# Performance work log

Measured on AMD Instinct MI355X. Metric: run time of the kernel, lower is better.

Reference implementation:

```python
import jax, jax.numpy as jnp
import numpy as np

N = 50000        # nodes
E = 800000       # edges (avg degree 16)
D_IN = 19        # in_channels(16) + 2 coords + 1 observed flag
H = 64           # graph_hidden
L = 3            # graph_layers
EPS = 1e-5       # BatchNorm eps


def setup_inputs() -> dict:
    key = jax.random.key(0)
    ks = jax.random.split(key, 12)
    s = 0.05
    x = jax.random.normal(ks[0], (N, D_IN), jnp.float32)
    edge_index = jax.random.randint(ks[1], (2, E), 0, N, dtype=jnp.int32)
    return {
        "x": x,
        "edge_index": edge_index,
        # input projection + input BN
        "w_in": jax.random.normal(ks[2], (D_IN, H), jnp.float32) * s,
        "b_in": jnp.zeros((H,), jnp.float32),
        "bn0_g": jnp.ones((H,), jnp.float32),
        "bn0_b": jnp.zeros((H,), jnp.float32),
        # per-layer SAGEConv: lin_l (aggregated neighbors, with bias), lin_r (self, no bias)
        "wl": jax.random.normal(ks[3], (L, H, H), jnp.float32) * s,
        "bl": jnp.zeros((L, H), jnp.float32),
        "wr": jax.random.normal(ks[4], (L, H, H), jnp.float32) * s,
        # per-layer BatchNorm affine
        "bn_g": jnp.ones((L, H), jnp.float32),
        "bn_b": jnp.zeros((L, H), jnp.float32),
    }


def _batchnorm(h, g, b):
    # training-mode BN over the node axis (biased variance, like torch)
    mu = h.mean(axis=0)
    var = h.var(axis=0)
    return (h - mu) * jax.lax.rsqrt(var + EPS) * g + b


def reference(x, edge_index, w_in, b_in, bn0_g, bn0_b, wl, bl, wr, bn_g, bn_b):
    src = edge_index[0]
    dst = edge_index[1]
    n = x.shape[0]

    # input_proj -> BN -> ReLU  (dropout is identity at inference)
    h = x @ w_in + b_in
    h = jax.nn.relu(_batchnorm(h, bn0_g, bn0_b))

    # in-degree for mean aggregation (computed once)
    deg = jax.ops.segment_sum(jnp.ones((src.shape[0],), h.dtype), dst, num_segments=n)
    denom = jnp.maximum(deg, 1.0)[:, None]

    for l in range(L):
        # SAGEConv(mean): gather source feats, segment-mean into targets
        msgs = h[src]                                        # [E, H] gather
        agg = jax.ops.segment_sum(msgs, dst, num_segments=n) / denom
        h_new = agg @ wl[l] + bl[l] + h @ wr[l]
        h_new = jax.nn.relu(_batchnorm(h_new, bn_g[l], bn_b[l]))
        h = h + h_new                                        # residual
    return h
```

## Files before the change

kernel.cpp:

```cpp
#include <hip/hip_runtime.h>
#include <hip/hip_bf16.h>

#define NODES 50000
#define EDGES 800000
#define DIN   19
#define HDIM  64
#define LAYERS 3
#define BN_EPS 1e-5f

#define NBINS 196
#define EPB   4096
#define NBLK  196

typedef __attribute__((ext_vector_type(4))) float f32x4;
typedef __attribute__((ext_vector_type(8))) short s16x8;

__device__ inline ushort bf16bits(float f) {
    __hip_bfloat16 h = __float2bfloat16(f);
    return *reinterpret_cast<ushort*>(&h);
}
__device__ inline float bf16lo(unsigned v) { return __uint_as_float(v << 16); }
__device__ inline float bf16hi(unsigned v) { return __uint_as_float(v & 0xFFFF0000u); }


__global__ __launch_bounds__(1024) void k_sortA(const int* __restrict__ src, const int* __restrict__ dst,
                                                int2* __restrict__ cb, int* __restrict__ bintot,
                                                unsigned* __restrict__ bbuf) {
    __shared__ int hist[256];
    __shared__ int cur[256];
    __shared__ int wsum4[4];
    __shared__ unsigned stage[EPB];
    int blk = blockIdx.x, t = threadIdx.x;
    int e0 = blk * EPB;
    int ne = min(EPB, EDGES - e0);
    int d[4]; unsigned pk[4];
    #pragma unroll
    for (int i = 0; i < 4; ++i) {
        int j = t + i * 1024;
        if (j < ne) {
            int dd = dst[e0 + j];
            d[i] = dd;
            pk[i] = ((unsigned)(dd & 255) << 24) | (unsigned)src[e0 + j];
        } else d[i] = -1;
    }
    if (t < 256) hist[t] = 0;
    __syncthreads();
    #pragma unroll
    for (int i = 0; i < 4; ++i)
        if (d[i] >= 0) atomicAdd(&hist[d[i] >> 8], 1);
    __syncthreads();
    int ln = t & 63, wv = t >> 6;
    int cntv = 0, inc = 0;
    if (t < 256) {
        cntv = hist[t];
        inc = cntv;
        #pragma unroll
        for (int s = 1; s < 64; s <<= 1) {
            int u = __shfl_up(inc, s);
            if (ln >= s) inc += u;
        }
        if (ln == 63) wsum4[wv] = inc;
    }
    __syncthreads();
    if (t < 256) {
        int woff = 0;
        #pragma unroll
        for (int i = 0; i < 4; ++i) if (i < wv) woff += wsum4[i];
        int excl = woff + inc - cntv;
        cur[t] = excl;
        if (t < NBINS) {
            cb[t * NBLK + blk] = make_int2(excl, cntv);
            if (cntv) atomicAdd(&bintot[t], cntv);
        }
    }
    __syncthreads();
    #pragma unroll
    for (int i = 0; i < 4; ++i)
        if (d[i] >= 0) {
            int slot = atomicAdd(&cur[d[i] >> 8], 1);
            stage[slot] = pk[i];
        }
    __syncthreads();
    #pragma unroll
    for (int i = 0; i < 4; ++i) {
        int j = t + i * 1024;
        if (j < ne) bbuf[e0 + j] = stage[j];
    }
}


__global__ __launch_bounds__(512) void k_binB(const int2* __restrict__ cb, const int* __restrict__ bintot,
                                              const unsigned* __restrict__ bbuf,
                                              int* __restrict__ off, float* __restrict__ rdenom,
                                              int* __restrict__ ebuf) {
    __shared__ int red[256];
    __shared__ int segoff[NBINS], segcnt[NBINS];
    __shared__ int deg[256], loff[256], cur[256];
    __shared__ int wsum4[4];
    __shared__ int binoff_s;
    int b = blockIdx.x, t = threadIdx.x;
    int ln = t & 63, wv = t >> 6;
    if (t < 256) red[t] = (t < b) ? bintot[t] : 0;
    __syncthreads();
    #pragma unroll
    for (int s = 128; s > 0; s >>= 1) {
        if (t < s && t + s < 256) red[t] += red[t + s];
        __syncthreads();
    }
    if (t == 0) binoff_s = red[0];
    if (t < NBINS) {
        int2 c = cb[b * NBLK + t];
        segoff[t] = c.x; segcnt[t] = c.y;
    }
    if (t < 256) { deg[t] = 0; cur[t] = 0; }
    __syncthreads();
    int binoff = binoff_s;
    for (int sg = wv; sg < NBLK; sg += 8) {
        int c = segcnt[sg];
        const unsigned* bp = bbuf + sg * EPB + segoff[sg];
        for (int k = ln; k < c; k += 64) atomicAdd(&deg[bp[k] >> 24], 1);
    }
    __syncthreads();
    int dv = 0, inc = 0;
    if (t < 256) {
        dv = deg[t];
        inc = dv;
        #pragma unroll
        for (int s = 1; s < 64; s <<= 1) {
            int u = __shfl_up(inc, s);
            if (ln >= s) inc += u;
        }
        if (ln == 63) wsum4[wv] = inc;
    }
    __syncthreads();
    if (t < 256) {
        int woff = 0;
        #pragma unroll
        for (int i = 0; i < 4; ++i) if (i < wv) woff += wsum4[i];
        int excl = woff + inc - dv;
        loff[t] = excl;
        int node = (b << 8) + t;
        if (node < NODES) {
            off[node] = binoff + excl;
            rdenom[node] = 1.0f / fmaxf((float)dv, 1.0f);
        }
        if (b == NBINS - 1 && t == 0) off[NODES] = EDGES;
    }
    __syncthreads();
    for (int sg = wv; sg < NBLK; sg += 8) {
        int c = segcnt[sg];
        const unsigned* bp = bbuf + sg * EPB + segoff[sg];
        for (int k = ln; k < c; k += 64) {
            unsigned e = bp[k];
            int dd = e >> 24;
            int slot = atomicAdd(&cur[dd], 1);
            ebuf[binoff + loff[dd] + slot] = (int)(e & 0xFFFFFFu);
        }
    }
}


__global__ void k_prep(const float* __restrict__ x, const float* __restrict__ w_in,
                       const float* __restrict__ wl, const float* __restrict__ wr,
                       __hip_bfloat16* __restrict__ xpad, __hip_bfloat16* __restrict__ WiT,
                       __hip_bfloat16* __restrict__ WcatT) {
    int i = blockIdx.x * blockDim.x + threadIdx.x;
    if (i < 64 * 32) {
        int c = i >> 5, k = i & 31;
        WiT[i] = __float2bfloat16(k < DIN ? w_in[k * HDIM + c] : 0.0f);
    }
    if (i < LAYERS * 64 * 128) {
        int l = i >> 13;
        int rem = i & 8191;
        int c = rem >> 7, k = rem & 127;
        float v = (k < 64) ? wl[(l * 64 + k) * 64 + c] : wr[(l * 64 + (k - 64)) * 64 + c];
        WcatT[i] = __float2bfloat16(v);
    }
    if (i < NODES * 32) {
        int n = i >> 5, k = i & 31;
        xpad[i] = __float2bfloat16(k < DIN ? x[n * DIN + k] : 0.0f);
    }
}


__global__ void k_gemm(const __hip_bfloat16* __restrict__ A, int lda,
                       const __hip_bfloat16* __restrict__ WT, int K,
                       const float* __restrict__ bias, ushort* __restrict__ tb,
                       float* __restrict__ stats) {
    __shared__ float red[4][128];
    int lane = threadIdx.x & 63, wave = threadIdx.x >> 6;
    int row0 = blockIdx.x * 64 + wave * 16;
    int r = lane & 15, g = lane >> 4;
    f32x4 acc[4] = {{0.f,0.f,0.f,0.f},{0.f,0.f,0.f,0.f},{0.f,0.f,0.f,0.f},{0.f,0.f,0.f,0.f}};
    int ar = row0 + r;
    if (ar >= NODES) ar = NODES - 1;
    for (int k0 = 0; k0 < K; k0 += 32) {
        s16x8 af = *(const s16x8*)(A + (size_t)ar * lda + k0 + g * 8);
        #pragma unroll
        for (int j = 0; j < 4; ++j) {
            s16x8 bf = *(const s16x8*)(WT + (size_t)(j * 16 + r) * K + k0 + g * 8);
            acc[j] = __builtin_amdgcn_mfma_f32_16x16x32_bf16(af, bf, acc[j], 0, 0, 0);
        }
    }
    float s_[4], q_[4];
    #pragma unroll
    for (int j = 0; j < 4; ++j) {
        float b = bias[j * 16 + r];
        float s = 0.0f, q = 0.0f;
        #pragma unroll
        for (int i = 0; i < 4; ++i) {
            int row = row0 + g * 4 + i;
            if (row < NODES) {
                float v = acc[j][i] + b;
                tb[(size_t)row * 64 + j * 16 + r] = bf16bits(v);
                s += v; q += v * v;
            }
        }
        s += __shfl_xor(s, 16); s += __shfl_xor(s, 32);
        q += __shfl_xor(q, 16); q += __shfl_xor(q, 32);
        s_[j] = s; q_[j] = q;
    }
    if (g == 0) {
        #pragma unroll
        for (int j = 0; j < 4; ++j) {
            red[wave][j * 16 + r] = s_[j];
            red[wave][64 + j * 16 + r] = q_[j];
        }
    }
    __syncthreads();
    if (threadIdx.x < 128) {
        float tot = red[0][threadIdx.x] + red[1][threadIdx.x] +
                    red[2][threadIdx.x] + red[3][threadIdx.x];
        atomicAdd(&stats[threadIdx.x * 16], tot);
    }
}


__global__ void k_apply(const ushort* __restrict__ tb, const float* __restrict__ stats,
                        const float* __restrict__ gamma, const float* __restrict__ beta,
                        float* __restrict__ h, __hip_bfloat16* __restrict__ AB, int residual) {
    int idx0 = blockIdx.x * blockDim.x + threadIdx.x;
    int stride = gridDim.x * blockDim.x;
    const float invN = 1.0f / NODES;
    for (int idx = idx0; idx < NODES * 16; idx += stride) {
        int n = idx >> 4;
        int j = (idx & 15) * 4;
        ushort4 tv = *(const ushort4*)(tb + (size_t)n * 64 + j);
        float tf[4] = { __uint_as_float((unsigned)tv.x << 16), __uint_as_float((unsigned)tv.y << 16),
                        __uint_as_float((unsigned)tv.z << 16), __uint_as_float((unsigned)tv.w << 16) };
        f32x4 hv;
        if (residual) hv = *(const f32x4*)(h + (size_t)n * 64 + j);
        float out[4];
        ushort ub[4];
        #pragma unroll
        for (int k = 0; k < 4; ++k) {
            int f = j + k;
            float mu = stats[f * 16] * invN;
            float var = stats[(64 + f) * 16] * invN - mu * mu;
            float sc = gamma[f] * rsqrtf(var + BN_EPS);
            float sh = beta[f] - mu * sc;
            float v = fmaxf(tf[k] * sc + sh, 0.0f);
            out[k] = residual ? (hv[k] + v) : v;
            ub[k] = bf16bits(out[k]);
        }
        *(f32x4*)(h + (size_t)n * 64 + j) = f32x4{out[0], out[1], out[2], out[3]};
        *(ushort4*)((ushort*)AB + (size_t)n * 128 + 64 + j) = make_ushort4(ub[0], ub[1], ub[2], ub[3]);
    }
}


__global__ void k_agg(const int* __restrict__ off, const int* __restrict__ ebuf,
                      const float* __restrict__ rdenom, __hip_bfloat16* __restrict__ ABh) {
    unsigned* AB = (unsigned*)ABh;
    int lane = threadIdx.x & 63;
    int half = lane >> 5;
    int fl = lane & 31;
    int w = blockIdx.x * (blockDim.x >> 6) + (threadIdx.x >> 6);
    int nw = gridDim.x * (blockDim.x >> 6);
    for (int n = w; n < NODES; n += nw) {
        int p0 = off[n], p1 = off[n + 1];
        float a0 = 0.0f, a1 = 0.0f;
        int p = p0 + half;
        for (; p + 6 < p1; p += 8) {
            int s0 = ebuf[p];
            int s1 = ebuf[p + 2];
            int s2 = ebuf[p + 4];
            int s3 = ebuf[p + 6];
            unsigned v0 = AB[(size_t)s0 * 64 + 32 + fl];
            unsigned v1 = AB[(size_t)s1 * 64 + 32 + fl];
            unsigned v2 = AB[(size_t)s2 * 64 + 32 + fl];
            unsigned v3 = AB[(size_t)s3 * 64 + 32 + fl];
            a0 += bf16lo(v0); a1 += bf16hi(v0);
            a0 += bf16lo(v1); a1 += bf16hi(v1);
            a0 += bf16lo(v2); a1 += bf16hi(v2);
            a0 += bf16lo(v3); a1 += bf16hi(v3);
        }
        for (; p < p1; p += 2) {
            int s = ebuf[p];
            unsigned v = AB[(size_t)s * 64 + 32 + fl];
            a0 += bf16lo(v); a1 += bf16hi(v);
        }
        a0 += __shfl_xor(a0, 32);
        a1 += __shfl_xor(a1, 32);
        if (half == 0) {
            float rd = rdenom[n];
            unsigned o = (unsigned)bf16bits(a0 * rd) | ((unsigned)bf16bits(a1 * rd) << 16);
            AB[(size_t)n * 64 + fl] = o;
        }
    }
}


extern "C" void kernel_launch(void* const* d_in, const int* in_sizes, int n_in,
                              void* d_out, int out_size, void* d_ws, size_t ws_size,
                              hipStream_t stream) {
    const float* x    = (const float*)d_in[0];
    const int*   ei   = (const int*)d_in[1];
    const float* w_in = (const float*)d_in[2];
    const float* b_in = (const float*)d_in[3];
    const float* bn0g = (const float*)d_in[4];
    const float* bn0b = (const float*)d_in[5];
    const float* wl   = (const float*)d_in[6];
    const float* bl   = (const float*)d_in[7];
    const float* wr   = (const float*)d_in[8];
    const float* bng  = (const float*)d_in[9];
    const float* bnb  = (const float*)d_in[10];
    const int* esrc = ei;
    const int* edst = ei + EDGES;
    float* h = (float*)d_out;

    char* p = (char*)d_ws;
    auto alloc = [&](size_t bytes) {
        char* r = p;
        p += (bytes + 255) & ~size_t(255);
        return r;
    };
    int*   bintot = (int*)alloc((size_t)NBINS * 4);
    float* stats  = (float*)alloc((size_t)4 * 128 * 16 * 4);
    char*  zero_end = p;
    int2*     cb   = (int2*)alloc((size_t)NBINS * NBLK * 8);
    unsigned* bbuf = (unsigned*)alloc((size_t)NBLK * EPB * 4);
    int*   off  = (int*)alloc((size_t)(NODES + 1) * 4);
    float* rden = (float*)alloc((size_t)NODES * 4);
    int*   ebuf = (int*)alloc((size_t)EDGES * 4);
    __hip_bfloat16* xpad  = (__hip_bfloat16*)alloc((size_t)NODES * 32 * 2);
    __hip_bfloat16* WiT   = (__hip_bfloat16*)alloc(64 * 32 * 2);
    __hip_bfloat16* WcatT = (__hip_bfloat16*)alloc(LAYERS * 64 * 128 * 2);
    __hip_bfloat16* AB    = (__hip_bfloat16*)alloc((size_t)NODES * 128 * 2);
    ushort* tb = (ushort*)alloc((size_t)NODES * 64 * 2);

    hipMemsetAsync(bintot, 0, (size_t)(zero_end - (char*)bintot), stream);

    k_sortA<<<NBLK, 1024, 0, stream>>>(esrc, edst, cb, bintot, bbuf);
    k_binB<<<NBINS, 512, 0, stream>>>(cb, bintot, bbuf, off, rden, ebuf);
    k_prep<<<(NODES * 32 + 255) / 256, 256, 0, stream>>>(x, w_in, wl, wr, xpad, WiT, WcatT);

    k_gemm<<<(NODES + 63) / 64, 256, 0, stream>>>(xpad, 32, WiT, 32, b_in, tb, stats);
    k_apply<<<2048, 256, 0, stream>>>(tb, stats, bn0g, bn0b, h, AB, 0);

    for (int l = 0; l < LAYERS; ++l) {
        k_agg<<<2048, 256, 0, stream>>>(off, ebuf, rden, AB);
        k_gemm<<<(NODES + 63) / 64, 256, 0, stream>>>(AB, 128, WcatT + l * 8192, 128,
                                                      bl + l * 64, tb, stats + (l + 1) * 2048);
        k_apply<<<2048, 256, 0, stream>>>(tb, stats + (l + 1) * 2048, bng + l * 64, bnb + l * 64,
                                          h, AB, 1);
    }
}
```

Measured before the change: 304.8 us.

## Fuse pipeline into persistent megakernel with grid barriers and LDS-resident aggregation

Result: slower. 683.4 us (+124.2%).

```diff
diff --git a/kernel.cpp b/kernel.cpp
--- a/kernel.cpp
+++ b/kernel.cpp
@@ -4,13 +4,15 @@
 #define NODES 50000
 #define EDGES 800000
 #define DIN   19
-#define HDIM  64
 #define LAYERS 3
 #define BN_EPS 1e-5f
 
 #define NBINS 196
-#define EPB   4096
-#define NBLK  196
+#define EPB   2048
+#define NBLK  391
+#define NTILES 782
+#define GRID  782
+#define TPB   256
 
 typedef __attribute__((ext_vector_type(4))) float f32x4;
 typedef __attribute__((ext_vector_type(8))) short s16x8;
@@ -22,180 +24,243 @@
 __device__ inline float bf16lo(unsigned v) { return __uint_as_float(v << 16); }
 __device__ inline float bf16hi(unsigned v) { return __uint_as_float(v & 0xFFFF0000u); }
 
-
-__global__ __launch_bounds__(1024) void k_sortA(const int* __restrict__ src, const int* __restrict__ dst,
-                                                int2* __restrict__ cb, int* __restrict__ bintot,
-                                                unsigned* __restrict__ bbuf) {
-    __shared__ int hist[256];
-    __shared__ int cur[256];
-    __shared__ int wsum4[4];
-    __shared__ unsigned stage[EPB];
-    int blk = blockIdx.x, t = threadIdx.x;
-    int e0 = blk * EPB;
+union SMem {
+    struct { int hist[256], cur[256], wsum[4]; unsigned stage[EPB]; } sort;
+    struct { int red[256]; int segoff[NBLK], segcnt[NBLK], pre[NBLK + 1];
+             int deg[256], loff[256], cur[256], wsum[4]; } binb;
+    struct { ushort aggtile[64][136]; float red[4][128]; } gemm;
+};
+
+__device__ inline void gbar(int* barr, int k) {
+    __syncthreads();
+    if (threadIdx.x == 0) {
+        __threadfence();
+        __hip_atomic_fetch_add(&barr[(blockIdx.x & 7) * 16], 1,
+                               __ATOMIC_RELEASE, __HIP_MEMORY_SCOPE_AGENT);
+        if (blockIdx.x == 0) {
+            const int target = (k + 1) * GRID;
+            for (;;) {
+                int s = 0;
+                #pragma unroll
+                for (int i = 0; i < 8; ++i)
+                    s += __hip_atomic_load(&barr[i * 16], __ATOMIC_RELAXED, __HIP_MEMORY_SCOPE_AGENT);
+                if (s >= target) break;
+                __builtin_amdgcn_s_sleep(4);
+            }
+            __hip_atomic_fetch_add(&barr[128], 1, __ATOMIC_RELEASE, __HIP_MEMORY_SCOPE_AGENT);
+        } else {
+            while (__hip_atomic_load(&barr[128], __ATOMIC_RELAXED, __HIP_MEMORY_SCOPE_AGENT) < k + 1)
+                __builtin_amdgcn_s_sleep(16);
+        }
+        __threadfence();
+    }
+    __syncthreads();
+}
+
+
+__device__ inline void do_sort(int c, int t, const int* __restrict__ esrc,
+                               const int* __restrict__ edst, int2* __restrict__ cb,
+                               int* __restrict__ bintot, unsigned* __restrict__ bbuf, SMem& sm) {
+    int ln = t & 63, wv = t >> 6;
+    int e0 = c * EPB;
     int ne = min(EPB, EDGES - e0);
-    int d[4]; unsigned pk[4];
-    #pragma unroll
-    for (int i = 0; i < 4; ++i) {
-        int j = t + i * 1024;
+    int d[8]; unsigned pk[8];
+    #pragma unroll
+    for (int i = 0; i < 8; ++i) {
+        int j = t + i * TPB;
         if (j < ne) {
-            int dd = dst[e0 + j];
+            int dd = edst[e0 + j];
             d[i] = dd;
-            pk[i] = ((unsigned)(dd & 255) << 24) | (unsigned)src[e0 + j];
+            pk[i] = ((unsigned)(dd & 255) << 24) | (unsigned)esrc[e0 + j];
         } else d[i] = -1;
     }
-    if (t < 256) hist[t] = 0;
-    __syncthreads();
-    #pragma unroll
-    for (int i = 0; i < 4; ++i)
-        if (d[i] >= 0) atomicAdd(&hist[d[i] >> 8], 1);
-    __syncthreads();
+    sm.sort.hist[t] = 0;
+    __syncthreads();
+    #pragma unroll
+    for (int i = 0; i < 8; ++i)
+        if (d[i] >= 0) atomicAdd(&sm.sort.hist[d[i] >> 8], 1);
+    __syncthreads();
+    int cnt = sm.sort.hist[t], inc = cnt;
+    #pragma unroll
+    for (int s = 1; s < 64; s <<= 1) {
+        int u = __shfl_up(inc, s);
+        if (ln >= s) inc += u;
+    }
+    if (ln == 63) sm.sort.wsum[wv] = inc;
+    __syncthreads();
+    int woff = 0;
+    #pragma unroll
+    for (int i = 0; i < 4; ++i) if (i < wv) woff += sm.sort.wsum[i];
+    int excl = woff + inc - cnt;
+    sm.sort.cur[t] = excl;
+    if (t < NBINS) {
+        cb[t * NBLK + c] = make_int2(excl, cnt);
+        if (cnt) atomicAdd(&bintot[t], cnt);
+    }
+    __syncthreads();
+    #pragma unroll
+    for (int i = 0; i < 8; ++i)
+        if (d[i] >= 0) {
+            int slot = atomicAdd(&sm.sort.cur[d[i] >> 8], 1);
+            sm.sort.stage[slot] = pk[i];
+        }
+    __syncthreads();
+    #pragma unroll
+    for (int i = 0; i < 8; ++i) {
+        int j = t + i * TPB;
+        if (j < ne) bbuf[e0 + j] = sm.sort.stage[j];
+    }
+    __syncthreads();
+}
+
+
+__device__ inline int ubound(const int* pre, int f) {
+    int lo = 0, hi = NBLK;
+    while (lo + 1 < hi) {
+        int mid = (lo + hi) >> 1;
+        if (pre[mid] <= f) lo = mid; else hi = mid;
+    }
+    return lo;
+}
+
+__device__ inline void do_binb(int b, int t, const int2* __restrict__ cb,
+                               const int* __restrict__ bintot, const unsigned* __restrict__ bbuf,
+                               int* __restrict__ off, float* __restrict__ rden,
+                               int* __restrict__ ebuf, SMem& sm) {
     int ln = t & 63, wv = t >> 6;
-    int cntv = 0, inc = 0;
-    if (t < 256) {
-        cntv = hist[t];
-        inc = cntv;
-        #pragma unroll
-        for (int s = 1; s < 64; s <<= 1) {
-            int u = __shfl_up(inc, s);
-            if (ln >= s) inc += u;
-        }
-        if (ln == 63) wsum4[wv] = inc;
-    }
-    __syncthreads();
-    if (t < 256) {
-        int woff = 0;
-        #pragma unroll
-        for (int i = 0; i < 4; ++i) if (i < wv) woff += wsum4[i];
-        int excl = woff + inc - cntv;
-        cur[t] = excl;
-        if (t < NBINS) {
-            cb[t * NBLK + blk] = make_int2(excl, cntv);
-            if (cntv) atomicAdd(&bintot[t], cntv);
-        }
-    }
-    __syncthreads();
-    #pragma unroll
-    for (int i = 0; i < 4; ++i)
-        if (d[i] >= 0) {
-            int slot = atomicAdd(&cur[d[i] >> 8], 1);
-            stage[slot] = pk[i];
-        }
-    __syncthreads();
-    #pragma unroll
-    for (int i = 0; i < 4; ++i) {
-        int j = t + i * 1024;
-        if (j < ne) bbuf[e0 + j] = stage[j];
-    }
-}
-
-
-__global__ __launch_bounds__(512) void k_binB(const int2* __restrict__ cb, const int* __restrict__ bintot,
-                                              const unsigned* __restrict__ bbuf,
-                                              int* __restrict__ off, float* __restrict__ rdenom,
-                                              int* __restrict__ ebuf) {
-    __shared__ int red[256];
-    __shared__ int segoff[NBINS], segcnt[NBINS];
-    __shared__ int deg[256], loff[256], cur[256];
-    __shared__ int wsum4[4];
-    __shared__ int binoff_s;
-    int b = blockIdx.x, t = threadIdx.x;
-    int ln = t & 63, wv = t >> 6;
-    if (t < 256) red[t] = (t < b) ? bintot[t] : 0;
+    sm.binb.red[t] = (t < b) ? bintot[t] : 0;
     __syncthreads();
     #pragma unroll
     for (int s = 128; s > 0; s >>= 1) {
-        if (t < s && t + s < 256) red[t] += red[t + s];
+        if (t < s) sm.binb.red[t] += sm.binb.red[t + s];
         __syncthreads();
     }
-    if (t == 0) binoff_s = red[0];
-    if (t < NBINS) {
-        int2 c = cb[b * NBLK + t];
-        segoff[t] = c.x; segcnt[t] = c.y;
-    }
-    if (t < 256) { deg[t] = 0; cur[t] = 0; }
-    __syncthreads();
-    int binoff = binoff_s;
-    for (int sg = wv; sg < NBLK; sg += 8) {
-        int c = segcnt[sg];
-        const unsigned* bp = bbuf + sg * EPB + segoff[sg];
-        for (int k = ln; k < c; k += 64) atomicAdd(&deg[bp[k] >> 24], 1);
-    }
-    __syncthreads();
-    int dv = 0, inc = 0;
-    if (t < 256) {
-        dv = deg[t];
-        inc = dv;
-        #pragma unroll
-        for (int s = 1; s < 64; s <<= 1) {
-            int u = __shfl_up(inc, s);
-            if (ln >= s) inc += u;
-        }
-        if (ln == 63) wsum4[wv] = inc;
-    }
-    __syncthreads();
-    if (t < 256) {
-        int woff = 0;
-        #pragma unroll
-        for (int i = 0; i < 4; ++i) if (i < wv) woff += wsum4[i];
-        int excl = woff + inc - dv;
-        loff[t] = excl;
-        int node = (b << 8) + t;
-        if (node < NODES) {
-            off[node] = binoff + excl;
-            rdenom[node] = 1.0f / fmaxf((float)dv, 1.0f);
-        }
-        if (b == NBINS - 1 && t == 0) off[NODES] = EDGES;
-    }
-    __syncthreads();
-    for (int sg = wv; sg < NBLK; sg += 8) {
-        int c = segcnt[sg];
-        const unsigned* bp = bbuf + sg * EPB + segoff[sg];
-        for (int k = ln; k < c; k += 64) {
-            unsigned e = bp[k];
-            int dd = e >> 24;
-            int slot = atomicAdd(&cur[dd], 1);
-            ebuf[binoff + loff[dd] + slot] = (int)(e & 0xFFFFFFu);
-        }
-    }
-}
-
-
-__global__ void k_prep(const float* __restrict__ x, const float* __restrict__ w_in,
-                       const float* __restrict__ wl, const float* __restrict__ wr,
-                       __hip_bfloat16* __restrict__ xpad, __hip_bfloat16* __restrict__ WiT,
-                       __hip_bfloat16* __restrict__ WcatT) {
-    int i = blockIdx.x * blockDim.x + threadIdx.x;
-    if (i < 64 * 32) {
-        int c = i >> 5, k = i & 31;
-        WiT[i] = __float2bfloat16(k < DIN ? w_in[k * HDIM + c] : 0.0f);
-    }
-    if (i < LAYERS * 64 * 128) {
-        int l = i >> 13;
-        int rem = i & 8191;
-        int c = rem >> 7, k = rem & 127;
-        float v = (k < 64) ? wl[(l * 64 + k) * 64 + c] : wr[(l * 64 + (k - 64)) * 64 + c];
-        WcatT[i] = __float2bfloat16(v);
-    }
-    if (i < NODES * 32) {
-        int n = i >> 5, k = i & 31;
-        xpad[i] = __float2bfloat16(k < DIN ? x[n * DIN + k] : 0.0f);
-    }
-}
-
-
-__global__ void k_gemm(const __hip_bfloat16* __restrict__ A, int lda,
-                       const __hip_bfloat16* __restrict__ WT, int K,
-                       const float* __restrict__ bias, ushort* __restrict__ tb,
-                       float* __restrict__ stats) {
-    __shared__ float red[4][128];
-    int lane = threadIdx.x & 63, wave = threadIdx.x >> 6;
-    int row0 = blockIdx.x * 64 + wave * 16;
+    int binoff = sm.binb.red[0];
+    for (int sg = t; sg < NBLK; sg += TPB) {
+        int2 c = cb[b * NBLK + sg];
+        sm.binb.segoff[sg] = c.x;
+        sm.binb.segcnt[sg] = c.y;
+    }
+    sm.binb.deg[t] = 0;
+    sm.binb.cur[t] = 0;
+    __syncthreads();
+    if (wv == 0) {
+        int carry = 0;
+        for (int base = 0; base < NBLK; base += 64) {
+            int idx = base + ln;
+            int v = (idx < NBLK) ? sm.binb.segcnt[idx] : 0;
+            int inc = v;
+            #pragma unroll
+            for (int s = 1; s < 64; s <<= 1) {
+                int u = __shfl_up(inc, s);
+                if (ln >= s) inc += u;
+            }
+            if (idx < NBLK) sm.binb.pre[idx] = carry + inc - v;
+            carry += __shfl(inc, 63);
+        }
+        if (ln == 0) sm.binb.pre[NBLK] = carry;
+    }
+    __syncthreads();
+    int total = sm.binb.pre[NBLK];
+    for (int f = t; f < total; f += TPB) {
+        int sg = ubound(sm.binb.pre, f);
+        unsigned e = bbuf[sg * EPB + sm.binb.segoff[sg] + (f - sm.binb.pre[sg])];
+        atomicAdd(&sm.binb.deg[e >> 24], 1);
+    }
+    __syncthreads();
+    int dv = sm.binb.deg[t], inc2 = dv;
+    #pragma unroll
+    for (int s = 1; s < 64; s <<= 1) {
+        int u = __shfl_up(inc2, s);
+        if (ln >= s) inc2 += u;
+    }
+    if (ln == 63) sm.binb.wsum[wv] = inc2;
+    __syncthreads();
+    int woff = 0;
+    #pragma unroll
+    for (int i = 0; i < 4; ++i) if (i < wv) woff += sm.binb.wsum[i];
+    int excl = woff + inc2 - dv;
+    sm.binb.loff[t] = excl;
+    int node = (b << 8) + t;
+    if (node < NODES) {
+        off[node] = binoff + excl;
+        rden[node] = 1.0f / fmaxf((float)dv, 1.0f);
+    }
+    if (b == NBINS - 1 && t == 0) off[NODES] = EDGES;
+    __syncthreads();
+    for (int f = t; f < total; f += TPB) {
+        int sg = ubound(sm.binb.pre, f);
+        unsigned e = bbuf[sg * EPB + sm.binb.segoff[sg] + (f - sm.binb.pre[sg])];
+        int dd = e >> 24;
+        int slot = atomicAdd(&sm.binb.cur[dd], 1);
+        ebuf[binoff + sm.binb.loff[dd] + slot] = (int)(e & 0xFFFFFFu);
+    }
+    __syncthreads();
+}
+
+
+__device__ inline void do_agg(int rb, int t, const int* __restrict__ off,
+                              const int* __restrict__ ebuf, const float* __restrict__ rden,
+                              const ushort* __restrict__ hb, SMem& sm) {
+    const unsigned* HB = (const unsigned*)hb;
+    unsigned (*AG)[68] = (unsigned (*)[68])sm.gemm.aggtile;
+    int lane = t & 63, wave = t >> 6;
+    int half = lane >> 5, fl = lane & 31;
+    #pragma unroll 1
+    for (int i = 0; i < 16; ++i) {
+        int n = rb * 64 + wave * 16 + i;
+        if (n < NODES) {
+            int p0 = off[n], p1 = off[n + 1];
+            float a0 = 0.0f, a1 = 0.0f;
+            int p = p0 + half;
+            for (; p + 6 < p1; p += 8) {
+                int s0 = ebuf[p], s1 = ebuf[p + 2], s2 = ebuf[p + 4], s3 = ebuf[p + 6];
+                unsigned v0 = HB[(size_t)s0 * 32 + fl];
+                unsigned v1 = HB[(size_t)s1 * 32 + fl];
+                unsigned v2 = HB[(size_t)s2 * 32 + fl];
+                unsigned v3 = HB[(size_t)s3 * 32 + fl];
+                a0 += bf16lo(v0); a1 += bf16hi(v0);
+                a0 += bf16lo(v1); a1 += bf16hi(v1);
+                a0 += bf16lo(v2); a1 += bf16hi(v2);
+                a0 += bf16lo(v3); a1 += bf16hi(v3);
+            }
+            for (; p < p1; p += 2) {
+                unsigned v = HB[(size_t)ebuf[p] * 32 + fl];
+                a0 += bf16lo(v); a1 += bf16hi(v);
+            }
+            a0 += __shfl_xor(a0, 32);
+            a1 += __shfl_xor(a1, 32);
+            if (half == 0) {
+                float rd = rden[n];
+                AG[wave * 16 + i][fl] =
+                    (unsigned)bf16bits(a0 * rd) | ((unsigned)bf16bits(a1 * rd) << 16);
+            }
+        }
+    }
+    __syncthreads();
+}
+
+
+template<int K, bool ALDS>
+__device__ inline void do_gemm(int rb, int t, const ushort* __restrict__ Aglob,
+                               const ushort* __restrict__ WT, const float* __restrict__ bias,
+                               ushort* __restrict__ tb, float* __restrict__ stats,
+                               const ushort* __restrict__ hb, SMem& sm) {
+    int lane = t & 63, wave = t >> 6;
+    int row0 = rb * 64 + wave * 16;
     int r = lane & 15, g = lane >> 4;
     f32x4 acc[4] = {{0.f,0.f,0.f,0.f},{0.f,0.f,0.f,0.f},{0.f,0.f,0.f,0.f},{0.f,0.f,0.f,0.f}};
     int ar = row0 + r;
     if (ar >= NODES) ar = NODES - 1;
+    #pragma unroll
     for (int k0 = 0; k0 < K; k0 += 32) {
-        s16x8 af = *(const s16x8*)(A + (size_t)ar * lda + k0 + g * 8);
+        s16x8 af;
+        if (ALDS) {
+            if (k0 < 64) af = *(const s16x8*)&sm.gemm.aggtile[wave * 16 + r][k0 + g * 8];
+            else         af = *(const s16x8*)(hb + (size_t)ar * 64 + (k0 - 64) + g * 8);
+        } else {
+            af = *(const s16x8*)(Aglob + (size_t)ar * 32 + k0 + g * 8);
+        }
         #pragma unroll
         for (int j = 0; j < 4; ++j) {
             s16x8 bf = *(const s16x8*)(WT + (size_t)(j * 16 + r) * K + k0 + g * 8);
@@ -223,26 +288,26 @@
     if (g == 0) {
         #pragma unroll
         for (int j = 0; j < 4; ++j) {
-            red[wave][j * 16 + r] = s_[j];
-            red[wave][64 + j * 16 + r] = q_[j];
-        }
-    }
-    __syncthreads();
-    if (threadIdx.x < 128) {
-        float tot = red[0][threadIdx.x] + red[1][threadIdx.x] +
-                    red[2][threadIdx.x] + red[3][threadIdx.x];
-        atomicAdd(&stats[threadIdx.x * 16], tot);
-    }
-}
-
-
-__global__ void k_apply(const ushort* __restrict__ tb, const float* __restrict__ stats,
-                        const float* __restrict__ gamma, const float* __restrict__ beta,
-                        float* __restrict__ h, __hip_bfloat16* __restrict__ AB, int residual) {
-    int idx0 = blockIdx.x * blockDim.x + threadIdx.x;
-    int stride = gridDim.x * blockDim.x;
+            sm.gemm.red[wave][j * 16 + r] = s_[j];
+            sm.gemm.red[wave][64 + j * 16 + r] = q_[j];
+        }
+    }
+    __syncthreads();
+    if (t < 128) {
+        float tot = sm.gemm.red[0][t] + sm.gemm.red[1][t] +
+                    sm.gemm.red[2][t] + sm.gemm.red[3][t];
+        atomicAdd(&stats[t * 16], tot);
+    }
+    __syncthreads();
+}
+
+
+__device__ inline void do_apply(int t, const ushort* __restrict__ tb,
+                                const float* __restrict__ stats, const float* __restrict__ gamma,
+                                const float* __restrict__ beta, float* __restrict__ h,
+                                ushort* __restrict__ hb, bool residual) {
     const float invN = 1.0f / NODES;
-    for (int idx = idx0; idx < NODES * 16; idx += stride) {
+    for (int idx = blockIdx.x * TPB + t; idx < NODES * 16; idx += GRID * TPB) {
         int n = idx >> 4;
         int j = (idx & 15) * 4;
         ushort4 tv = *(const ushort4*)(tb + (size_t)n * 64 + j);
@@ -264,49 +329,71 @@
             ub[k] = bf16bits(out[k]);
         }
         *(f32x4*)(h + (size_t)n * 64 + j) = f32x4{out[0], out[1], out[2], out[3]};
-        *(ushort4*)((ushort*)AB + (size_t)n * 128 + 64 + j) = make_ushort4(ub[0], ub[1], ub[2], ub[3]);
-    }
-}
-
-
-__global__ void k_agg(const int* __restrict__ off, const int* __restrict__ ebuf,
-                      const float* __restrict__ rdenom, __hip_bfloat16* __restrict__ ABh) {
-    unsigned* AB = (unsigned*)ABh;
-    int lane = threadIdx.x & 63;
-    int half = lane >> 5;
-    int fl = lane & 31;
-    int w = blockIdx.x * (blockDim.x >> 6) + (threadIdx.x >> 6);
-    int nw = gridDim.x * (blockDim.x >> 6);
-    for (int n = w; n < NODES; n += nw) {
-        int p0 = off[n], p1 = off[n + 1];
-        float a0 = 0.0f, a1 = 0.0f;
-        int p = p0 + half;
-        for (; p + 6 < p1; p += 8) {
-            int s0 = ebuf[p];
-            int s1 = ebuf[p + 2];
-            int s2 = ebuf[p + 4];
-            int s3 = ebuf[p + 6];
-            unsigned v0 = AB[(size_t)s0 * 64 + 32 + fl];
-            unsigned v1 = AB[(size_t)s1 * 64 + 32 + fl];
-            unsigned v2 = AB[(size_t)s2 * 64 + 32 + fl];
-            unsigned v3 = AB[(size_t)s3 * 64 + 32 + fl];
-            a0 += bf16lo(v0); a1 += bf16hi(v0);
-            a0 += bf16lo(v1); a1 += bf16hi(v1);
-            a0 += bf16lo(v2); a1 += bf16hi(v2);
-            a0 += bf16lo(v3); a1 += bf16hi(v3);
-        }
-        for (; p < p1; p += 2) {
-            int s = ebuf[p];
-            unsigned v = AB[(size_t)s * 64 + 32 + fl];
-            a0 += bf16lo(v); a1 += bf16hi(v);
-        }
-        a0 += __shfl_xor(a0, 32);
-        a1 += __shfl_xor(a1, 32);
-        if (half == 0) {
-            float rd = rdenom[n];
-            unsigned o = (unsigned)bf16bits(a0 * rd) | ((unsigned)bf16bits(a1 * rd) << 16);
-            AB[(size_t)n * 64 + fl] = o;
-        }
+        *(ushort4*)(hb + (size_t)n * 64 + j) = make_ushort4(ub[0], ub[1], ub[2], ub[3]);
+    }
+}
+
+
+__global__ void k_first(const float* __restrict__ x, const float* __restrict__ w_in,
+                        const float* __restrict__ wl, const float* __restrict__ wr,
+                        ushort* __restrict__ xpad, ushort* __restrict__ WiT,
+                        ushort* __restrict__ WcatT, int* __restrict__ barr,
+                        int* __restrict__ bintot, float* __restrict__ stats) {
+    int i0 = blockIdx.x * blockDim.x + threadIdx.x;
+    int stride = gridDim.x * blockDim.x;
+    for (int i = i0; i < 256; i += stride) barr[i] = 0;
+    for (int i = i0; i < NBINS; i += stride) bintot[i] = 0;
+    for (int i = i0; i < 4 * 2048; i += stride) stats[i] = 0.0f;
+    for (int i = i0; i < 64 * 32; i += stride) {
+        int c = i >> 5, k = i & 31;
+        WiT[i] = bf16bits(k < DIN ? w_in[k * 64 + c] : 0.0f);
+    }
+    for (int i = i0; i < LAYERS * 64 * 128; i += stride) {
+        int l = i >> 13, rem = i & 8191;
+        int c = rem >> 7, k = rem & 127;
+        float v = (k < 64) ? wl[(l * 64 + k) * 64 + c] : wr[(l * 64 + (k - 64)) * 64 + c];
+        WcatT[i] = bf16bits(v);
+    }
+    for (int i = i0; i < NODES * 32; i += stride) {
+        int n = i >> 5, k = i & 31;
+        xpad[i] = bf16bits(k < DIN ? x[n * DIN + k] : 0.0f);
+    }
+}
+
+
+__global__ __launch_bounds__(TPB, 4) void k_mega(
+    const int* __restrict__ esrc, const int* __restrict__ edst,
+    const float* __restrict__ b_in, const float* __restrict__ bn0g, const float* __restrict__ bn0b,
+    const float* __restrict__ bl, const float* __restrict__ bng, const float* __restrict__ bnb,
+    const ushort* __restrict__ xpad, const ushort* __restrict__ WiT, const ushort* __restrict__ WcatT,
+    int2* __restrict__ cb, int* __restrict__ bintot, unsigned* __restrict__ bbuf,
+    int* __restrict__ off, float* __restrict__ rden, int* __restrict__ ebuf,
+    ushort* __restrict__ tb, ushort* __restrict__ hb, float* __restrict__ stats,
+    float* __restrict__ h, int* __restrict__ barr) {
+    __shared__ SMem sm;
+    int t = threadIdx.x;
+    int bk = 0;
+
+    for (int c = blockIdx.x; c < NBLK; c += GRID)
+        do_sort(c, t, esrc, edst, cb, bintot, bbuf, sm);
+    gbar(barr, bk++);
+
+    if (blockIdx.x < NBINS)
+        do_binb(blockIdx.x, t, cb, bintot, bbuf, off, rden, ebuf, sm);
+    __syncthreads();
+    do_gemm<32, false>(blockIdx.x, t, xpad, WiT, b_in, tb, stats, nullptr, sm);
+    gbar(barr, bk++);
+
+    do_apply(t, tb, stats, bn0g, bn0b, h, hb, false);
+    gbar(barr, bk++);
+
+    for (int l = 0; l < LAYERS; ++l) {
+        do_agg(blockIdx.x, t, off, ebuf, rden, hb, sm);
+        do_gemm<128, true>(blockIdx.x, t, nullptr, WcatT + l * 8192, bl + l * 64,
+                           tb, stats + (l + 1) * 2048, hb, sm);
+        gbar(barr, bk++);
+        do_apply(t, tb, stats + (l + 1) * 2048, bng + l * 64, bnb + l * 64, h, hb, true);
+        if (l < LAYERS - 1) gbar(barr, bk++);
     }
 }
 
@@ -335,34 +422,22 @@
         p += (bytes + 255) & ~size_t(255);
         return r;
     };
-    int*   bintot = (int*)alloc((size_t)NBINS * 4);
-    float* stats  = (float*)alloc((size_t)4 * 128 * 16 * 4);
-    char*  zero_end = p;
-    int2*     cb   = (int2*)alloc((size_t)NBINS * NBLK * 8);
-    unsigned* bbuf = (unsigned*)alloc((size_t)NBLK * EPB * 4);
-    int*   off  = (int*)alloc((size_t)(NODES + 1) * 4);
-    float* rden = (float*)alloc((size_t)NODES * 4);
-    int*   ebuf = (int*)alloc((size_t)EDGES * 4);
-    __hip_bfloat16* xpad  = (__hip_bfloat16*)alloc((size_t)NODES * 32 * 2);
-    __hip_bfloat16* WiT   = (__hip_bfloat16*)alloc(64 * 32 * 2);
-    __hip_bfloat16* WcatT = (__hip_bfloat16*)alloc(LAYERS * 64 * 128 * 2);
-    __hip_bfloat16* AB    = (__hip_bfloat16*)alloc((size_t)NODES * 128 * 2);
-    ushort* tb = (ushort*)alloc((size_t)NODES * 64 * 2);
-
-    hipMemsetAsync(bintot, 0, (size_t)(zero_end - (char*)bintot), stream);
-
-    k_sortA<<<NBLK, 1024, 0, stream>>>(esrc, edst, cb, bintot, bbuf);
-    k_binB<<<NBINS, 512, 0, stream>>>(cb, bintot, bbuf, off, rden, ebuf);
-    k_prep<<<(NODES * 32 + 255) / 256, 256, 0, stream>>>(x, w_in, wl, wr, xpad, WiT, WcatT);
-
-    k_gemm<<<(NODES + 63) / 64, 256, 0, stream>>>(xpad, 32, WiT, 32, b_in, tb, stats);
-    k_apply<<<2048, 256, 0, stream>>>(tb, stats, bn0g, bn0b, h, AB, 0);
-
-    for (int l = 0; l < LAYERS; ++l) {
-        k_agg<<<2048, 256, 0, stream>>>(off, ebuf, rden, AB);
-        k_gemm<<<(NODES + 63) / 64, 256, 0, stream>>>(AB, 128, WcatT + l * 8192, 128,
-                                                      bl + l * 64, tb, stats + (l + 1) * 2048);
-        k_apply<<<2048, 256, 0, stream>>>(tb, stats + (l + 1) * 2048, bng + l * 64, bnb + l * 64,
-                                          h, AB, 1);
-    }
-}
+    int*      barr   = (int*)alloc(1024);
+    int*      bintot = (int*)alloc((size_t)NBINS * 4);
+    float*    stats  = (float*)alloc((size_t)4 * 2048 * 4);
+    int2*     cb     = (int2*)alloc((size_t)NBINS * NBLK * 8);
+    unsigned* bbuf   = (unsigned*)alloc((size_t)NBLK * EPB * 4);
+    int*      off    = (int*)alloc((size_t)(NODES + 1) * 4);
+    float*    rden   = (float*)alloc((size_t)NODES * 4);
+    int*      ebuf   = (int*)alloc((size_t)EDGES * 4);
+    ushort*   xpad   = (ushort*)alloc((size_t)NODES * 32 * 2);
+    ushort*   WiT    = (ushort*)alloc(64 * 32 * 2);
+    ushort*   WcatT  = (ushort*)alloc(LAYERS * 64 * 128 * 2);
+    ushort*   tb     = (ushort*)alloc((size_t)NODES * 64 * 2);
+    ushort*   hb     = (ushort*)alloc((size_t)NODES * 64 * 2);
+
+    k_first<<<512, TPB, 0, stream>>>(x, w_in, wl, wr, xpad, WiT, WcatT, barr, bintot, stats);
+    k_mega<<<GRID, TPB, 0, stream>>>(esrc, edst, b_in, bn0g, bn0b, bl, bng, bnb,
+                                     xpad, WiT, WcatT, cb, bintot, bbuf, off, rden, ebuf,
+                                     tb, hb, stats, h, barr);
+}
```

## Fuse neighbor aggregation into layer GEMM and restructure edge binning and prep

Applied to the files above, without the earlier changes.

Result: slower. 360.8 us (+18.4%).

```diff
diff --git a/kernel.cpp b/kernel.cpp
--- a/kernel.cpp
+++ b/kernel.cpp
@@ -4,13 +4,14 @@
 #define NODES 50000
 #define EDGES 800000
 #define DIN   19
-#define HDIM  64
 #define LAYERS 3
 #define BN_EPS 1e-5f
 
 #define NBINS 196
 #define EPB   4096
 #define NBLK  196
+#define NTILES 782
+#define TPB   256
 
 typedef __attribute__((ext_vector_type(4))) float f32x4;
 typedef __attribute__((ext_vector_type(8))) short s16x8;
@@ -21,6 +22,27 @@
 }
 __device__ inline float bf16lo(unsigned v) { return __uint_as_float(v << 16); }
 __device__ inline float bf16hi(unsigned v) { return __uint_as_float(v & 0xFFFF0000u); }
+
+
+__global__ void k_wprep(const float* __restrict__ w_in, const float* __restrict__ wl,
+                        const float* __restrict__ wr, ushort* __restrict__ WiT,
+                        ushort* __restrict__ WcatT, int* __restrict__ bintot,
+                        float* __restrict__ stats) {
+    int i0 = blockIdx.x * blockDim.x + threadIdx.x;
+    int stride = gridDim.x * blockDim.x;
+    for (int i = i0; i < NBINS; i += stride) bintot[i] = 0;
+    for (int i = i0; i < 4 * 2048; i += stride) stats[i] = 0.0f;
+    for (int i = i0; i < 64 * 32; i += stride) {
+        int c = i >> 5, k = i & 31;
+        WiT[i] = bf16bits(k < DIN ? w_in[k * 64 + c] : 0.0f);
+    }
+    for (int i = i0; i < LAYERS * 64 * 128; i += stride) {
+        int l = i >> 13, rem = i & 8191;
+        int c = rem >> 7, k = rem & 127;
+        float v = (k < 64) ? wl[(l * 64 + k) * 64 + c] : wr[(l * 64 + (k - 64)) * 64 + c];
+        WcatT[i] = bf16bits(v);
+    }
+}
 
 
 __global__ __launch_bounds__(1024) void k_sortA(const int* __restrict__ src, const int* __restrict__ dst,
@@ -89,119 +111,98 @@
 }
 
 
-__global__ __launch_bounds__(512) void k_binB(const int2* __restrict__ cb, const int* __restrict__ bintot,
+__device__ inline int ubound(const int* pre, int f) {
+    int lo = 0, hi = NBLK;
+    while (lo + 1 < hi) {
+        int mid = (lo + hi) >> 1;
+        if (pre[mid] <= f) lo = mid; else hi = mid;
+    }
+    return lo;
+}
+
+__global__ __launch_bounds__(TPB) void k_binB(const int2* __restrict__ cb, const int* __restrict__ bintot,
                                               const unsigned* __restrict__ bbuf,
-                                              int* __restrict__ off, float* __restrict__ rdenom,
+                                              int* __restrict__ off, float* __restrict__ rden,
                                               int* __restrict__ ebuf) {
     __shared__ int red[256];
-    __shared__ int segoff[NBINS], segcnt[NBINS];
+    __shared__ int segoff[NBLK], segcnt[NBLK], pre[NBLK + 1];
     __shared__ int deg[256], loff[256], cur[256];
     __shared__ int wsum4[4];
-    __shared__ int binoff_s;
     int b = blockIdx.x, t = threadIdx.x;
     int ln = t & 63, wv = t >> 6;
-    if (t < 256) red[t] = (t < b) ? bintot[t] : 0;
+    red[t] = (t < b) ? bintot[t] : 0;
     __syncthreads();
     #pragma unroll
     for (int s = 128; s > 0; s >>= 1) {
-        if (t < s && t + s < 256) red[t] += red[t + s];
+        if (t < s) red[t] += red[t + s];
         __syncthreads();
     }
-    if (t == 0) binoff_s = red[0];
-    if (t < NBINS) {
+    int binoff = red[0];
+    if (t < NBLK) {
         int2 c = cb[b * NBLK + t];
         segoff[t] = c.x; segcnt[t] = c.y;
     }
-    if (t < 256) { deg[t] = 0; cur[t] = 0; }
-    __syncthreads();
-    int binoff = binoff_s;
-    for (int sg = wv; sg < NBLK; sg += 8) {
-        int c = segcnt[sg];
-        const unsigned* bp = bbuf + sg * EPB + segoff[sg];
-        for (int k = ln; k < c; k += 64) atomicAdd(&deg[bp[k] >> 24], 1);
-    }
-    __syncthreads();
-    int dv = 0, inc = 0;
-    if (t < 256) {
-        dv = deg[t];
-        inc = dv;
-        #pragma unroll
-        for (int s = 1; s < 64; s <<= 1) {
-            int u = __shfl_up(inc, s);
-            if (ln >= s) inc += u;
-        }
-        if (ln == 63) wsum4[wv] = inc;
-    }
-    __syncthreads();
-    if (t < 256) {
-        int woff = 0;
-        #pragma unroll
-        for (int i = 0; i < 4; ++i) if (i < wv) woff += wsum4[i];
-        int excl = woff + inc - dv;
-        loff[t] = excl;
-        int node = (b << 8) + t;
-        if (node < NODES) {
-            off[node] = binoff + excl;
-            rdenom[node] = 1.0f / fmaxf((float)dv, 1.0f);
-        }
-        if (b == NBINS - 1 && t == 0) off[NODES] = EDGES;
-    }
-    __syncthreads();
-    for (int sg = wv; sg < NBLK; sg += 8) {
-        int c = segcnt[sg];
-        const unsigned* bp = bbuf + sg * EPB + segoff[sg];
-        for (int k = ln; k < c; k += 64) {
-            unsigned e = bp[k];
-            int dd = e >> 24;
-            int slot = atomicAdd(&cur[dd], 1);
-            ebuf[binoff + loff[dd] + slot] = (int)(e & 0xFFFFFFu);
-        }
-    }
-}
-
-
-__global__ void k_prep(const float* __restrict__ x, const float* __restrict__ w_in,
-                       const float* __restrict__ wl, const float* __restrict__ wr,
-                       __hip_bfloat16* __restrict__ xpad, __hip_bfloat16* __restrict__ WiT,
-                       __hip_bfloat16* __restrict__ WcatT) {
-    int i = blockIdx.x * blockDim.x + threadIdx.x;
-    if (i < 64 * 32) {
-        int c = i >> 5, k = i & 31;
-        WiT[i] = __float2bfloat16(k < DIN ? w_in[k * HDIM + c] : 0.0f);
-    }
-    if (i < LAYERS * 64 * 128) {
-        int l = i >> 13;
-        int rem = i & 8191;
-        int c = rem >> 7, k = rem & 127;
-        float v = (k < 64) ? wl[(l * 64 + k) * 64 + c] : wr[(l * 64 + (k - 64)) * 64 + c];
-        WcatT[i] = __float2bfloat16(v);
-    }
-    if (i < NODES * 32) {
-        int n = i >> 5, k = i & 31;
-        xpad[i] = __float2bfloat16(k < DIN ? x[n * DIN + k] : 0.0f);
-    }
-}
-
-
-__global__ void k_gemm(const __hip_bfloat16* __restrict__ A, int lda,
-                       const __hip_bfloat16* __restrict__ WT, int K,
-                       const float* __restrict__ bias, ushort* __restrict__ tb,
-                       float* __restrict__ stats) {
-    __shared__ float red[4][128];
-    int lane = threadIdx.x & 63, wave = threadIdx.x >> 6;
-    int row0 = blockIdx.x * 64 + wave * 16;
+    deg[t] = 0; cur[t] = 0;
+    __syncthreads();
+    if (wv == 0) {
+        int carry = 0;
+        for (int base = 0; base < NBLK; base += 64) {
+            int idx = base + ln;
+            int v = (idx < NBLK) ? segcnt[idx] : 0;
+            int inc = v;
+            #pragma unroll
+            for (int s = 1; s < 64; s <<= 1) {
+                int u = __shfl_up(inc, s);
+                if (ln >= s) inc += u;
+            }
+            if (idx < NBLK) pre[idx] = carry + inc - v;
+            carry += __shfl(inc, 63);
+        }
+        if (ln == 0) pre[NBLK] = carry;
+    }
+    __syncthreads();
+    int total = pre[NBLK];
+    for (int f = t; f < total; f += TPB) {
+        int sg = ubound(pre, f);
+        unsigned e = bbuf[sg * EPB + segoff[sg] + (f - pre[sg])];
+        atomicAdd(&deg[e >> 24], 1);
+    }
+    __syncthreads();
+    int dv = deg[t], inc2 = dv;
+    #pragma unroll
+    for (int s = 1; s < 64; s <<= 1) {
+        int u = __shfl_up(inc2, s);
+        if (ln >= s) inc2 += u;
+    }
+    if (ln == 63) wsum4[wv] = inc2;
+    __syncthreads();
+    int woff = 0;
+    #pragma unroll
+    for (int i = 0; i < 4; ++i) if (i < wv) woff += wsum4[i];
+    int excl = woff + inc2 - dv;
+    loff[t] = excl;
+    int node = (b << 8) + t;
+    if (node < NODES) {
+        off[node] = binoff + excl;
+        rden[node] = 1.0f / fmaxf((float)dv, 1.0f);
+    }
+    if (b == NBINS - 1 && t == 0) off[NODES] = EDGES;
+    __syncthreads();
+    for (int f = t; f < total; f += TPB) {
+        int sg = ubound(pre, f);
+        unsigned e = bbuf[sg * EPB + segoff[sg] + (f - pre[sg])];
+        int dd = e >> 24;
+        int slot = atomicAdd(&cur[dd], 1);
+        ebuf[binoff + loff[dd] + slot] = (int)(e & 0xFFFFFFu);
+    }
+}
+
+
+__device__ inline void gemm_epilogue(int t, int row0, f32x4* acc, const float* __restrict__ bias,
+                                     ushort* __restrict__ tb, float* __restrict__ stats,
+                                     float (*red)[128]) {
+    int lane = t & 63, wave = t >> 6;
     int r = lane & 15, g = lane >> 4;
-    f32x4 acc[4] = {{0.f,0.f,0.f,0.f},{0.f,0.f,0.f,0.f},{0.f,0.f,0.f,0.f},{0.f,0.f,0.f,0.f}};
-    int ar = row0 + r;
-    if (ar >= NODES) ar = NODES - 1;
-    for (int k0 = 0; k0 < K; k0 += 32) {
-        s16x8 af = *(const s16x8*)(A + (size_t)ar * lda + k0 + g * 8);
-        #pragma unroll
-        for (int j = 0; j < 4; ++j) {
-            s16x8 bf = *(const s16x8*)(WT + (size_t)(j * 16 + r) * K + k0 + g * 8);
-            acc[j] = __builtin_amdgcn_mfma_f32_16x16x32_bf16(af, bf, acc[j], 0, 0, 0);
-        }
-    }
     float s_[4], q_[4];
     #pragma unroll
     for (int j = 0; j < 4; ++j) {
@@ -209,7 +210,7 @@
         float s = 0.0f, q = 0.0f;
         #pragma unroll
         for (int i = 0; i < 4; ++i) {
-            int row = row0 + g * 4 + i;
+            int row = row0 + wave * 16 + g * 4 + i;
             if (row < NODES) {
                 float v = acc[j][i] + b;
                 tb[(size_t)row * 64 + j * 16 + r] = bf16bits(v);
@@ -228,17 +229,110 @@
         }
     }
     __syncthreads();
-    if (threadIdx.x < 128) {
-        float tot = red[0][threadIdx.x] + red[1][threadIdx.x] +
-                    red[2][threadIdx.x] + red[3][threadIdx.x];
-        atomicAdd(&stats[threadIdx.x * 16], tot);
-    }
+    if (t < 128) {
+        float tot = red[0][t] + red[1][t] + red[2][t] + red[3][t];
+        atomicAdd(&stats[t * 16], tot);
+    }
+}
+
+
+__global__ __launch_bounds__(TPB) void k_gemm0(const float* __restrict__ x, const ushort* __restrict__ WiT,
+                                               const float* __restrict__ bias, ushort* __restrict__ tb,
+                                               float* __restrict__ stats) {
+    __shared__ ushort xt[64][40];
+    __shared__ float red[4][128];
+    int t = threadIdx.x, rb = blockIdx.x;
+    int row0 = rb * 64;
+    int nv = min(64, NODES - row0);
+    unsigned* xz = (unsigned*)xt;
+    for (int i = t; i < 64 * 20; i += TPB) xz[i] = 0;
+    __syncthreads();
+    const float* xs = x + (size_t)row0 * DIN;
+    for (int e = t; e < nv * DIN; e += TPB) {
+        int n = e / DIN, k = e - n * DIN;
+        xt[n][k] = bf16bits(xs[e]);
+    }
+    __syncthreads();
+    int lane = t & 63, wave = t >> 6;
+    int r = lane & 15, g = lane >> 4;
+    f32x4 acc[4] = {{0.f,0.f,0.f,0.f},{0.f,0.f,0.f,0.f},{0.f,0.f,0.f,0.f},{0.f,0.f,0.f,0.f}};
+    s16x8 af = *(const s16x8*)&xt[wave * 16 + r][g * 8];
+    #pragma unroll
+    for (int j = 0; j < 4; ++j) {
+        s16x8 bf = *(const s16x8*)(WiT + (size_t)(j * 16 + r) * 32 + g * 8);
+        acc[j] = __builtin_amdgcn_mfma_f32_16x16x32_bf16(af, bf, acc[j], 0, 0, 0);
+    }
+    gemm_epilogue(t, row0, acc, bias, tb, stats, red);
+}
+
+
+__global__ __launch_bounds__(TPB) void k_aggemm(const int* __restrict__ off, const int* __restrict__ ebuf,
+                                                const float* __restrict__ rden, const ushort* __restrict__ hb,
+                                                const ushort* __restrict__ WT, const float* __restrict__ bias,
+                                                ushort* __restrict__ tb, float* __restrict__ stats) {
+    __shared__ ushort aggt[64][136];
+    __shared__ float red[4][128];
+    int t = threadIdx.x, rb = blockIdx.x;
+    const unsigned* HB = (const unsigned*)hb;
+    unsigned (*AG)[68] = (unsigned (*)[68])aggt;
+    int lane = t & 63, wave = t >> 6;
+    int half = lane >> 5, fl = lane & 31;
+    #pragma unroll 1
+    for (int i = 0; i < 16; ++i) {
+        int n = rb * 64 + wave * 16 + i;
+        if (n < NODES) {
+            int p0 = off[n], p1 = off[n + 1];
+            float a0 = 0.0f, a1 = 0.0f;
+            int p = p0 + half;
+            for (; p + 6 < p1; p += 8) {
+                int s0 = ebuf[p], s1 = ebuf[p + 2], s2 = ebuf[p + 4], s3 = ebuf[p + 6];
+                unsigned v0 = HB[(size_t)s0 * 32 + fl];
+                unsigned v1 = HB[(size_t)s1 * 32 + fl];
+                unsigned v2 = HB[(size_t)s2 * 32 + fl];
+                unsigned v3 = HB[(size_t)s3 * 32 + fl];
+                a0 += bf16lo(v0); a1 += bf16hi(v0);
+                a0 += bf16lo(v1); a1 += bf16hi(v1);
+                a0 += bf16lo(v2); a1 += bf16hi(v2);
+                a0 += bf16lo(v3); a1 += bf16hi(v3);
+            }
+            for (; p < p1; p += 2) {
+                unsigned v = HB[(size_t)ebuf[p] * 32 + fl];
+                a0 += bf16lo(v); a1 += bf16hi(v);
+            }
+            a0 += __shfl_xor(a0, 32);
+            a1 += __shfl_xor(a1, 32);
+            if (half == 0) {
+                float rd = rden[n];
+                AG[wave * 16 + i][fl] =
+                    (unsigned)bf16bits(a0 * rd) | ((unsigned)bf16bits(a1 * rd) << 16);
+            }
+        }
+    }
+    __syncthreads();
+    int r = lane & 15, g = lane >> 4;
+    int row0 = rb * 64;
+    int ar = row0 + wave * 16 + r;
+    if (ar >= NODES) ar = NODES - 1;
+    f32x4 acc[4] = {{0.f,0.f,0.f,0.f},{0.f,0.f,0.f,0.f},{0.f,0.f,0.f,0.f},{0.f,0.f,0.f,0.f}};
+    #pragma unroll
+    for (int k0 = 0; k0 < 128; k0 += 32) {
+        s16x8 af;
+        if (k0 < 64) af = *(const s16x8*)&aggt[wave * 16 + r][k0 + g * 8];
+        else         af = *(const s16x8*)(hb + (size_t)ar * 64 + (k0 - 64) + g * 8);
+        #pragma unroll
+        for (int j = 0; j < 4; ++j) {
+            s16x8 bf = *(const s16x8*)(WT + (size_t)(j * 16 + r) * 128 + k0 + g * 8);
+            acc[j] = __builtin_amdgcn_mfma_f32_16x16x32_bf16(af, bf, acc[j], 0, 0, 0);
+        }
+    }
+    gemm_epilogue(t, row0, acc, bias, tb, stats, red);
 }
 
 
 __global__ void k_apply(const ushort* __restrict__ tb, const float* __restrict__ stats,
                         const float* __restrict__ gamma, const float* __restrict__ beta,
-                        float* __restrict__ h, __hip_bfloat16* __restrict__ AB, int residual) {
+                        float* __restrict__ h, ushort* __restrict__ hb,
+                        int residual, int write_hb) {
     int idx0 = blockIdx.x * blockDim.x + threadIdx.x;
     int stride = gridDim.x * blockDim.x;
     const float invN = 1.0f / NODES;
@@ -264,49 +358,8 @@
             ub[k] = bf16bits(out[k]);
         }
         *(f32x4*)(h + (size_t)n * 64 + j) = f32x4{out[0], out[1], out[2], out[3]};
-        *(ushort4*)((ushort*)AB + (size_t)n * 128 + 64 + j) = make_ushort4(ub[0], ub[1], ub[2], ub[3]);
-    }
-}
-
-
-__global__ void k_agg(const int* __restrict__ off, const int* __restrict__ ebuf,
-                      const float* __restrict__ rdenom, __hip_bfloat16* __restrict__ ABh) {
-    unsigned* AB = (unsigned*)ABh;
-    int lane = threadIdx.x & 63;
-    int half = lane >> 5;
-    int fl = lane & 31;
-    int w = blockIdx.x * (blockDim.x >> 6) + (threadIdx.x >> 6);
-    int nw = gridDim.x * (blockDim.x >> 6);
-    for (int n = w; n < NODES; n += nw) {
-        int p0 = off[n], p1 = off[n + 1];
-        float a0 = 0.0f, a1 = 0.0f;
-        int p = p0 + half;
-        for (; p + 6 < p1; p += 8) {
-            int s0 = ebuf[p];
-            int s1 = ebuf[p + 2];
-            int s2 = ebuf[p + 4];
-            int s3 = ebuf[p + 6];
-            unsigned v0 = AB[(size_t)s0 * 64 + 32 + fl];
-            unsigned v1 = AB[(size_t)s1 * 64 + 32 + fl];
-            unsigned v2 = AB[(size_t)s2 * 64 + 32 + fl];
-            unsigned v3 = AB[(size_t)s3 * 64 + 32 + fl];
-            a0 += bf16lo(v0); a1 += bf16hi(v0);
-            a0 += bf16lo(v1); a1 += bf16hi(v1);
-            a0 += bf16lo(v2); a1 += bf16hi(v2);
-            a0 += bf16lo(v3); a1 += bf16hi(v3);
-        }
-        for (; p < p1; p += 2) {
-            int s = ebuf[p];
-            unsigned v = AB[(size_t)s * 64 + 32 + fl];
-            a0 += bf16lo(v); a1 += bf16hi(v);
-        }
-        a0 += __shfl_xor(a0, 32);
-        a1 += __shfl_xor(a1, 32);
-        if (half == 0) {
-            float rd = rdenom[n];
-            unsigned o = (unsigned)bf16bits(a0 * rd) | ((unsigned)bf16bits(a1 * rd) << 16);
-            AB[(size_t)n * 64 + fl] = o;
-        }
+        if (write_hb)
+            *(ushort4*)(hb + (size_t)n * 64 + j) = make_ushort4(ub[0], ub[1], ub[2], ub[3]);
     }
 }
 
@@ -335,34 +388,29 @@
         p += (bytes + 255) & ~size_t(255);
         return r;
     };
-    int*   bintot = (int*)alloc((size_t)NBINS * 4);
-    float* stats  = (float*)alloc((size_t)4 * 128 * 16 * 4);
-    char*  zero_end = p;
-    int2*     cb   = (int2*)alloc((size_t)NBINS * NBLK * 8);
-    unsigned* bbuf = (unsigned*)alloc((size_t)NBLK * EPB * 4);
-    int*   off  = (int*)alloc((size_t)(NODES + 1) * 4);
-    float* rden = (float*)alloc((size_t)NODES * 4);
-    int*   ebuf = (int*)alloc((size_t)EDGES * 4);
-    __hip_bfloat16* xpad  = (__hip_bfloat16*)alloc((size_t)NODES * 32 * 2);
-    __hip_bfloat16* WiT   = (__hip_bfloat16*)alloc(64 * 32 * 2);
-    __hip_bfloat16* WcatT = (__hip_bfloat16*)alloc(LAYERS * 64 * 128 * 2);
-    __hip_bfloat16* AB    = (__hip_bfloat16*)alloc((size_t)NODES * 128 * 2);
-    ushort* tb = (ushort*)alloc((size_t)NODES * 64 * 2);
-
-    hipMemsetAsync(bintot, 0, (size_t)(zero_end - (char*)bintot), stream);
-
+    int*      bintot = (int*)alloc((size_t)NBINS * 4);
+    float*    stats  = (float*)alloc((size_t)4 * 2048 * 4);
+    int2*     cb     = (int2*)alloc((size_t)NBINS * NBLK * 8);
+    unsigned* bbuf   = (unsigned*)alloc((size_t)NBLK * EPB * 4);
+    int*      off    = (int*)alloc((size_t)(NODES + 1) * 4);
+    float*    rden   = (float*)alloc((size_t)NODES * 4);
+    int*      ebuf   = (int*)alloc((size_t)EDGES * 4);
+    ushort*   WiT    = (ushort*)alloc(64 * 32 * 2);
+    ushort*   WcatT  = (ushort*)alloc(LAYERS * 64 * 128 * 2);
+    ushort*   tb     = (ushort*)alloc((size_t)NODES * 64 * 2);
+    ushort*   hb     = (ushort*)alloc((size_t)NODES * 64 * 2);
+
+    k_wprep<<<128, TPB, 0, stream>>>(w_in, wl, wr, WiT, WcatT, bintot, stats);
     k_sortA<<<NBLK, 1024, 0, stream>>>(esrc, edst, cb, bintot, bbuf);
-    k_binB<<<NBINS, 512, 0, stream>>>(cb, bintot, bbuf, off, rden, ebuf);
-    k_prep<<<(NODES * 32 + 255) / 256, 256, 0, stream>>>(x, w_in, wl, wr, xpad, WiT, WcatT);
-
-    k_gemm<<<(NODES + 63) / 64, 256, 0, stream>>>(xpad, 32, WiT, 32, b_in, tb, stats);
-    k_apply<<<2048, 256, 0, stream>>>(tb, stats, bn0g, bn0b, h, AB, 0);
+    k_binB<<<NBINS, TPB, 0, stream>>>(cb, bintot, bbuf, off, rden, ebuf);
+
+    k_gemm0<<<NTILES, TPB, 0, stream>>>(x, WiT, b_in, tb, stats);
+    k_apply<<<2048, TPB, 0, stream>>>(tb, stats, bn0g, bn0b, h, hb, 0, 1);
 
     for (int l = 0; l < LAYERS; ++l) {
-        k_agg<<<2048, 256, 0, stream>>>(off, ebuf, rden, AB);
-        k_gemm<<<(NODES + 63) / 64, 256, 0, stream>>>(AB, 128, WcatT + l * 8192, 128,
-                                                      bl + l * 64, tb, stats + (l + 1) * 2048);
-        k_apply<<<2048, 256, 0, stream>>>(tb, stats + (l + 1) * 2048, bng + l * 64, bnb + l * 64,
-                                          h, AB, 1);
-    }
-}
+        k_aggemm<<<NTILES, TPB, 0, stream>>>(off, ebuf, rden, hb, WcatT + l * 8192,
+                                             bl + l * 64, tb, stats + (l + 1) * 2048);
+        k_apply<<<2048, TPB, 0, stream>>>(tb, stats + (l + 1) * 2048, bng + l * 64, bnb + l * 64,
+                                          h, hb, 1, l < LAYERS - 1 ? 1 : 0);
+    }
+}
```
